# Kernel tuning notes

Measured on AMD Instinct MI355X. Metric: run time of the kernel, lower is better.

Reference implementation:

```python
import jax, jax.numpy as jnp
import numpy as np

N_BLOCKS = 64
BLOCK = 64
IN_SIZE = N_BLOCKS * BLOCK   # 4096
OUT_SIZE = N_BLOCKS * BLOCK  # 4096
EPS = 1e-6


def _masks():
    # block id per row/col (uniform block sizes)
    rb = np.repeat(np.arange(N_BLOCKS), BLOCK)
    cb = np.repeat(np.arange(N_BLOCKS), BLOCK)
    tree_mask = (rb[:, None] == cb[None, :]).astype(np.float32)    # block diagonal
    breeze_mask = (rb[:, None] < cb[None, :]).astype(np.float32)   # strict block upper-triangular
    return jnp.asarray(tree_mask), jnp.asarray(breeze_mask)


def setup_inputs() -> dict:
    key = jax.random.key(0)
    k1, k2, k3, k4 = jax.random.split(key, 4)
    x = jax.random.normal(k1, (8192, IN_SIZE), dtype=jnp.float32)
    x_init = jax.random.normal(k2, (8192, OUT_SIZE), dtype=jnp.float32)
    # inc_mode='no strict': treeWeights = sqrt(|randn| / sqrt(in_size/z_dim))
    tw = jnp.sqrt(jnp.abs(jax.random.normal(k3, (IN_SIZE, OUT_SIZE), dtype=jnp.float32))
                  / np.sqrt(IN_SIZE / N_BLOCKS))
    bbw = jax.random.normal(k4, (IN_SIZE, OUT_SIZE), dtype=jnp.float32) / np.sqrt(IN_SIZE)
    return {"x": x, "x_init": x_init, "treeWeights": tw, "breezeBiasWeights": bbw}


def reference(x, x_init, treeWeights, breezeBiasWeights):
    tree_mask, breeze_mask = _masks()
    # 'no strict': real weights are elementwise square (monotone-increasing, non-strict)
    tree_matrix = (treeWeights * treeWeights) * tree_mask          # [in, out]
    breeze_bias = x @ (breezeBiasWeights * breeze_mask)            # [B, out]
    h = x @ tree_matrix + x_init + breeze_bias                     # [B, out]
    # ActNorm-style data-dependent init (first call: bias/scale from batch stats)
    tree_bias = jax.lax.stop_gradient(jnp.mean(h, axis=0))         # [out]
    std = jax.lax.stop_gradient(jnp.std(h, axis=0))                # [out]
    tree_scale = jnp.sqrt(1.0 / (std + EPS))                       # stored scale; applied squared
    z = (h - tree_bias) * (tree_scale * tree_scale)
    return jax.nn.sigmoid(z)
```

## Files before the change

### kernel.cpp

```cpp
#include <hip/hip_runtime.h>
#include <stdint.h>


#define BATCH 8192
#define DIM   4096

typedef __bf16 v8bf __attribute__((ext_vector_type(8)));
typedef float  v4f  __attribute__((ext_vector_type(4)));

__device__ __forceinline__ unsigned short f2bf(float f) {
  unsigned int u = __float_as_uint(f);
  u += 0x7fffu + ((u >> 16) & 1u);
  return (unsigned short)(u >> 16);
}
__device__ __forceinline__ float bf2f(unsigned int h16) {
  return __uint_as_float(h16 << 16);
}

__device__ __forceinline__ void async_copy16(const void* g, void* l) {
  __builtin_amdgcn_global_load_lds(
      (__attribute__((address_space(1))) void*)g,
      (__attribute__((address_space(3))) void*)l, 16, 0, 0);
}

__global__ __launch_bounds__(256) void cvt_x_bf16(const float4* __restrict__ in,
                                                  uint4* __restrict__ out) {
  int i = blockIdx.x * 256 + threadIdx.x;
  float4 a = in[2 * i], b = in[2 * i + 1];
  uint4 o;
  o.x = (unsigned)f2bf(a.x) | ((unsigned)f2bf(a.y) << 16);
  o.y = (unsigned)f2bf(a.z) | ((unsigned)f2bf(a.w) << 16);
  o.z = (unsigned)f2bf(b.x) | ((unsigned)f2bf(b.y) << 16);
  o.w = (unsigned)f2bf(b.z) | ((unsigned)f2bf(b.w) << 16);
  out[i] = o;
}

__global__ __launch_bounds__(256) void build_Mt(const float* __restrict__ tw,
                                                const float* __restrict__ bbw,
                                                unsigned short* __restrict__ Mt) {
  const int kt = blockIdx.x, nt = blockIdx.y;
  const int t = threadIdx.x;
  const int jj = t & 63, i0 = t >> 6;
  __shared__ float tile[64 * 65];
  if (kt <= nt) {
    const bool diag = (kt == nt);
    const float* S = diag ? tw : bbw;
    #pragma unroll
    for (int r = 0; r < 16; ++r) {
      int i = i0 + r * 4;
      float v = S[(size_t)(kt * 64 + i) * DIM + nt * 64 + jj];
      tile[i * 65 + jj] = diag ? v * v : v;
    }
    __syncthreads();
    #pragma unroll
    for (int r = 0; r < 16; ++r) {
      int nl = i0 + r * 4;
      Mt[(size_t)(nt * 64 + nl) * DIM + kt * 64 + jj] = f2bf(tile[jj * 65 + nl]);
    }
  } else {
    #pragma unroll
    for (int r = 0; r < 16; ++r) {
      int nl = i0 + r * 4;
      Mt[(size_t)(nt * 64 + nl) * DIM + kt * 64 + jj] = 0;
    }
  }
}

__global__ __launch_bounds__(256) void gemm_tree(
    const unsigned short* __restrict__ Xb,
    const unsigned short* __restrict__ Mt,
    const float* __restrict__ Xi,
    unsigned short* __restrict__ H,
    float* __restrict__ colsum,
    float* __restrict__ colsumsq) {
  __shared__ unsigned short As[128 * 64];
  __shared__ unsigned short Bs[128 * 64];

  const int bid = (int)blockIdx.x;
  const int jc = 31 - (bid >> 6);
  const int bm = bid & 63;
  const int tid = threadIdx.x;
  const int wave = tid >> 6, lane = tid & 63;
  const int wm = (wave & 1) * 64, wn = (wave >> 1) * 64;
  const int lr = lane & 15, quad = lane >> 4;

  v4f acc[4][4];
  #pragma unroll
  for (int mi = 0; mi < 4; ++mi)
    #pragma unroll
    for (int ni = 0; ni < 4; ++ni) acc[mi][ni] = {0.f, 0.f, 0.f, 0.f};

  const int Kend = (jc + 1) * 128;
  const int srow = lane >> 3;
  const int scol = ((lane & 7) ^ srow) * 8;

  for (int k0 = 0; k0 < Kend; k0 += 64) {
    #pragma unroll
    for (int r = 0; r < 4; ++r) {
      int seg = wave * 4 + r;
      int row = seg * 8 + srow;
      const unsigned short* ga = Xb + (size_t)(bm * 128 + row) * DIM + (k0 + scol);
      const unsigned short* gb = Mt + (size_t)(jc * 128 + row) * DIM + (k0 + scol);
      async_copy16(ga, &As[seg * 512]);
      async_copy16(gb, &Bs[seg * 512]);
    }
    __syncthreads();
    #pragma unroll
    for (int kk = 0; kk < 2; ++kk) {
      const int sw = ((kk * 4 + quad) ^ (lr & 7)) * 8;
      v8bf a[4], b[4];
      #pragma unroll
      for (int mi = 0; mi < 4; ++mi)
        a[mi] = *(const v8bf*)&As[(wm + mi * 16 + lr) * 64 + sw];
      #pragma unroll
      for (int ni = 0; ni < 4; ++ni)
        b[ni] = *(const v8bf*)&Bs[(wn + ni * 16 + lr) * 64 + sw];
      #pragma unroll
      for (int mi = 0; mi < 4; ++mi)
        #pragma unroll
        for (int ni = 0; ni < 4; ++ni)
          acc[mi][ni] = __builtin_amdgcn_mfma_f32_16x16x32_bf16(
              a[mi], b[ni], acc[mi][ni], 0, 0, 0);
    }
    __syncthreads();
  }

  const int colT = jc * 128 + wn + lr;
  const int rowT = bm * 128 + wm + quad * 4;
  #pragma unroll
  for (int ni = 0; ni < 4; ++ni) {
    int col = colT + ni * 16;
    float s = 0.f, sq = 0.f;
    #pragma unroll
    for (int mi = 0; mi < 4; ++mi) {
      int row = rowT + mi * 16;
      #pragma unroll
      for (int r = 0; r < 4; ++r) {
        size_t idx = (size_t)(row + r) * DIM + col;
        float h = acc[mi][ni][r] + Xi[idx];
        H[idx] = f2bf(h);
        s += h;
        sq += h * h;
      }
    }
    s += __shfl_xor(s, 16);  s += __shfl_xor(s, 32);
    sq += __shfl_xor(sq, 16); sq += __shfl_xor(sq, 32);
    if (quad == 0) {
      atomicAdd(&colsum[col], s);
      atomicAdd(&colsumsq[col], sq);
    }
  }
}

__global__ __launch_bounds__(256) void finalize_stats(
    const float* __restrict__ colsum, const float* __restrict__ colsumsq,
    float* __restrict__ mean, float* __restrict__ scale) {
  int i = blockIdx.x * 256 + threadIdx.x;
  float m = colsum[i] * (1.0f / BATCH);
  float var = fmaxf(colsumsq[i] * (1.0f / BATCH) - m * m, 0.0f);
  mean[i] = m;
  scale[i] = 1.0f / (sqrtf(var) + 1e-6f);
}

__global__ __launch_bounds__(256) void norm_sigmoid(
    const uint4* __restrict__ H, const float* __restrict__ mean,
    const float* __restrict__ scale, float4* __restrict__ out) {
  int i = blockIdx.x * 256 + threadIdx.x;
  int cg = (i & 511) << 3;
  uint4 h = H[i];
  float4 m0 = *(const float4*)&mean[cg],  m1 = *(const float4*)&mean[cg + 4];
  float4 s0 = *(const float4*)&scale[cg], s1 = *(const float4*)&scale[cg + 4];
  float hv[8];
  hv[0] = bf2f(h.x & 0xffffu); hv[1] = bf2f(h.x >> 16);
  hv[2] = bf2f(h.y & 0xffffu); hv[3] = bf2f(h.y >> 16);
  hv[4] = bf2f(h.z & 0xffffu); hv[5] = bf2f(h.z >> 16);
  hv[6] = bf2f(h.w & 0xffffu); hv[7] = bf2f(h.w >> 16);
  float mm[8] = {m0.x, m0.y, m0.z, m0.w, m1.x, m1.y, m1.z, m1.w};
  float ss[8] = {s0.x, s0.y, s0.z, s0.w, s1.x, s1.y, s1.z, s1.w};
  #pragma unroll
  for (int j = 0; j < 8; ++j) {
    float z = (hv[j] - mm[j]) * ss[j];
    hv[j] = 1.0f / (1.0f + __expf(-z));
  }
  out[2 * i]     = make_float4(hv[0], hv[1], hv[2], hv[3]);
  out[2 * i + 1] = make_float4(hv[4], hv[5], hv[6], hv[7]);
}

extern "C" void kernel_launch(void* const* d_in, const int* in_sizes, int n_in,
                              void* d_out, int out_size, void* d_ws, size_t ws_size,
                              hipStream_t stream) {
  const float* x      = (const float*)d_in[0];
  const float* x_init = (const float*)d_in[1];
  const float* tw     = (const float*)d_in[2];
  const float* bbw    = (const float*)d_in[3];
  float* out = (float*)d_out;

  char* ws = (char*)d_ws;
  unsigned short* Xb = (unsigned short*)(ws);
  unsigned short* Mt = (unsigned short*)(ws + (size_t)67108864);
  unsigned short* H  = (unsigned short*)(ws + (size_t)100663296);
  float* colsum   = (float*)(ws + (size_t)167772160);
  float* colsumsq = (float*)(ws + (size_t)167772160 + 16384);
  float* mean     = (float*)(ws + (size_t)167772160 + 32768);
  float* scale    = (float*)(ws + (size_t)167772160 + 49152);

  hipMemsetAsync(colsum, 0, 32768, stream);

  cvt_x_bf16<<<(BATCH * DIM / 8 + 255) / 256, 256, 0, stream>>>(
      (const float4*)x, (uint4*)Xb);
  build_Mt<<<dim3(64, 64), 256, 0, stream>>>(tw, bbw, Mt);
  gemm_tree<<<2048, 256, 0, stream>>>(Xb, Mt, x_init, H, colsum, colsumsq);
  finalize_stats<<<16, 256, 0, stream>>>(colsum, colsumsq, mean, scale);
  norm_sigmoid<<<(BATCH * DIM / 8 + 255) / 256, 256, 0, stream>>>(
      (const uint4*)H, mean, scale, (float4*)out);
}
```

Baseline: 599.0 us.

## Double-buffer 256x256 GEMM tiles with paired triangular jobs and fused prep kernel

Rewrites the triangular GEMM to use 256x256 tiles with 8 waves and 32 accumulators per wave, and double-buffers the LDS loads so the next K tile is prefetched while MFMAs run. Each of the 256 workgroups takes two complementary column strips (jc and 15-jc) so every block does the same total K work. The bf16 conversion and weight-matrix build kernels are merged into one launch. The larger tiles raise register and LDS pressure, and a grid of only 256 blocks may leave some compute units idle.

```diff
diff --git a/kernel.cpp b/kernel.cpp
--- a/kernel.cpp
+++ b/kernel.cpp
@@ -23,131 +23,177 @@
       (__attribute__((address_space(3))) void*)l, 16, 0, 0);
 }
 
-__global__ __launch_bounds__(256) void cvt_x_bf16(const float4* __restrict__ in,
-                                                  uint4* __restrict__ out) {
-  int i = blockIdx.x * 256 + threadIdx.x;
-  float4 a = in[2 * i], b = in[2 * i + 1];
-  uint4 o;
-  o.x = (unsigned)f2bf(a.x) | ((unsigned)f2bf(a.y) << 16);
-  o.y = (unsigned)f2bf(a.z) | ((unsigned)f2bf(a.w) << 16);
-  o.z = (unsigned)f2bf(b.x) | ((unsigned)f2bf(b.y) << 16);
-  o.w = (unsigned)f2bf(b.z) | ((unsigned)f2bf(b.w) << 16);
-  out[i] = o;
-}
-
-__global__ __launch_bounds__(256) void build_Mt(const float* __restrict__ tw,
-                                                const float* __restrict__ bbw,
-                                                unsigned short* __restrict__ Mt) {
-  const int kt = blockIdx.x, nt = blockIdx.y;
-  const int t = threadIdx.x;
-  const int jj = t & 63, i0 = t >> 6;
+__global__ __launch_bounds__(256) void prep(
+    const float4* __restrict__ x, uint4* __restrict__ Xb,
+    const float* __restrict__ tw, const float* __restrict__ bbw,
+    unsigned short* __restrict__ Mt) {
+  const int b = (int)blockIdx.x;
+  const int t = (int)threadIdx.x;
   __shared__ float tile[64 * 65];
-  if (kt <= nt) {
-    const bool diag = (kt == nt);
-    const float* S = diag ? tw : bbw;
-    #pragma unroll
-    for (int r = 0; r < 16; ++r) {
-      int i = i0 + r * 4;
-      float v = S[(size_t)(kt * 64 + i) * DIM + nt * 64 + jj];
-      tile[i * 65 + jj] = diag ? v * v : v;
-    }
-    __syncthreads();
-    #pragma unroll
-    for (int r = 0; r < 16; ++r) {
-      int nl = i0 + r * 4;
-      Mt[(size_t)(nt * 64 + nl) * DIM + kt * 64 + jj] = f2bf(tile[jj * 65 + nl]);
-    }
+  if (b < 16384) {
+    int i = b * 256 + t;
+    float4 a = x[2 * i], c = x[2 * i + 1];
+    uint4 o;
+    o.x = (unsigned)f2bf(a.x) | ((unsigned)f2bf(a.y) << 16);
+    o.y = (unsigned)f2bf(a.z) | ((unsigned)f2bf(a.w) << 16);
+    o.z = (unsigned)f2bf(c.x) | ((unsigned)f2bf(c.y) << 16);
+    o.w = (unsigned)f2bf(c.z) | ((unsigned)f2bf(c.w) << 16);
+    Xb[i] = o;
   } else {
-    #pragma unroll
-    for (int r = 0; r < 16; ++r) {
-      int nl = i0 + r * 4;
-      Mt[(size_t)(nt * 64 + nl) * DIM + kt * 64 + jj] = 0;
+    const int bb = b - 16384;
+    const int kt = bb & 63, nt = bb >> 6;
+    const int jj = t & 63, i0 = t >> 6;
+    if (kt <= nt) {
+      const bool diag = (kt == nt);
+      const float* S = diag ? tw : bbw;
+      #pragma unroll
+      for (int r = 0; r < 16; ++r) {
+        int i = i0 + r * 4;
+        float v = S[(size_t)(kt * 64 + i) * DIM + nt * 64 + jj];
+        tile[i * 65 + jj] = diag ? v * v : v;
+      }
+      __syncthreads();
+      #pragma unroll
+      for (int r = 0; r < 16; ++r) {
+        int nl = i0 + r * 4;
+        Mt[(size_t)(nt * 64 + nl) * DIM + kt * 64 + jj] = f2bf(tile[jj * 65 + nl]);
+      }
+    } else {
+      #pragma unroll
+      for (int r = 0; r < 16; ++r) {
+        int nl = i0 + r * 4;
+        Mt[(size_t)(nt * 64 + nl) * DIM + kt * 64 + jj] = 0;
+      }
     }
   }
 }
 
-__global__ __launch_bounds__(256) void gemm_tree(
+__global__ __launch_bounds__(512, 2) void gemm_tree(
     const unsigned short* __restrict__ Xb,
     const unsigned short* __restrict__ Mt,
     const float* __restrict__ Xi,
     unsigned short* __restrict__ H,
     float* __restrict__ colsum,
     float* __restrict__ colsumsq) {
-  __shared__ unsigned short As[128 * 64];
-  __shared__ unsigned short Bs[128 * 64];
-
-  const int bid = (int)blockIdx.x;
-  const int jc = 31 - (bid >> 6);
-  const int bm = bid & 63;
-  const int tid = threadIdx.x;
+  __shared__ unsigned short As[2 * 16384];
+  __shared__ unsigned short Bs[2 * 16384];
+
+  const int b = (int)blockIdx.x;
+  const int p = b >> 5;
+  const int bm = b & 31;
+  const int tid = (int)threadIdx.x;
   const int wave = tid >> 6, lane = tid & 63;
-  const int wm = (wave & 1) * 64, wn = (wave >> 1) * 64;
+  const int wm = wave >> 2, wn = wave & 3;
   const int lr = lane & 15, quad = lane >> 4;
-
-  v4f acc[4][4];
-  #pragma unroll
-  for (int mi = 0; mi < 4; ++mi)
-    #pragma unroll
-    for (int ni = 0; ni < 4; ++ni) acc[mi][ni] = {0.f, 0.f, 0.f, 0.f};
-
-  const int Kend = (jc + 1) * 128;
   const int srow = lane >> 3;
   const int scol = ((lane & 7) ^ srow) * 8;
 
-  for (int k0 = 0; k0 < Kend; k0 += 64) {
+  const size_t abase = (size_t)(bm * 256 + wave * 8 + srow) * DIM + scol;
+
+  for (int job = 0; job < 2; ++job) {
+    const int jc = job ? p : 15 - p;
+    const int ntiles = (jc + 1) * 4;
+    const size_t bbase = (size_t)(jc * 256 + wave * 8 + srow) * DIM + scol;
+
+    v4f acc[8][4];
+    #pragma unroll
+    for (int mi = 0; mi < 8; ++mi)
+      #pragma unroll
+      for (int ni = 0; ni < 4; ++ni) acc[mi][ni] = {0.f, 0.f, 0.f, 0.f};
+
     #pragma unroll
     for (int r = 0; r < 4; ++r) {
-      int seg = wave * 4 + r;
-      int row = seg * 8 + srow;
-      const unsigned short* ga = Xb + (size_t)(bm * 128 + row) * DIM + (k0 + scol);
-      const unsigned short* gb = Mt + (size_t)(jc * 128 + row) * DIM + (k0 + scol);
-      async_copy16(ga, &As[seg * 512]);
-      async_copy16(gb, &Bs[seg * 512]);
-    }
-    __syncthreads();
+      async_copy16(Xb + abase + (size_t)(r * 64) * DIM, &As[(r * 8 + wave) * 512]);
+      async_copy16(Mt + bbase + (size_t)(r * 64) * DIM, &Bs[(r * 8 + wave) * 512]);
+    }
+
+    for (int t = 0; t < ntiles; ++t) {
+      const unsigned short* Ac = &As[(t & 1) * 16384];
+      const unsigned short* Bc = &Bs[(t & 1) * 16384];
+      const int nb = ((t + 1) & 1) * 16384;
+      const size_t nk = (size_t)(t + 1) * 64;
+      const bool pre = (t + 1 < ntiles);
+
+      if (pre) {
+        #pragma unroll
+        for (int r = 0; r < 2; ++r) {
+          async_copy16(Xb + abase + (size_t)(r * 64) * DIM + nk,
+                       &As[nb + (r * 8 + wave) * 512]);
+          async_copy16(Mt + bbase + (size_t)(r * 64) * DIM + nk,
+                       &Bs[nb + (r * 8 + wave) * 512]);
+        }
+        asm volatile("s_waitcnt vmcnt(4)" ::: "memory");
+      } else {
+        asm volatile("s_waitcnt vmcnt(0)" ::: "memory");
+      }
+      __builtin_amdgcn_s_barrier();
+      __builtin_amdgcn_sched_barrier(0);
+
+      v8bf bfr[4][2];
+      #pragma unroll
+      for (int ni = 0; ni < 4; ++ni)
+        #pragma unroll
+        for (int kk = 0; kk < 2; ++kk)
+          bfr[ni][kk] = *(const v8bf*)&Bc[(wn * 64 + ni * 16 + lr) * 64 +
+                                          (((kk * 4 + quad) ^ (lr & 7)) * 8)];
+
+      #pragma unroll
+      for (int q = 0; q < 4; ++q) {
+        v8bf afr[2][2];
+        #pragma unroll
+        for (int m2 = 0; m2 < 2; ++m2)
+          #pragma unroll
+          for (int kk = 0; kk < 2; ++kk)
+            afr[m2][kk] = *(const v8bf*)&Ac[(wm * 128 + (q * 2 + m2) * 16 + lr) * 64 +
+                                            (((kk * 4 + quad) ^ (lr & 7)) * 8)];
+        if (pre && q < 2) {
+          const int r = q + 2;
+          async_copy16(Xb + abase + (size_t)(r * 64) * DIM + nk,
+                       &As[nb + (r * 8 + wave) * 512]);
+          async_copy16(Mt + bbase + (size_t)(r * 64) * DIM + nk,
+                       &Bs[nb + (r * 8 + wave) * 512]);
+        }
+        __builtin_amdgcn_s_barrier();
+        __builtin_amdgcn_sched_barrier(0);
+        __builtin_amdgcn_s_setprio(1);
+        #pragma unroll
+        for (int kk = 0; kk < 2; ++kk)
+          #pragma unroll
+          for (int m2 = 0; m2 < 2; ++m2)
+            #pragma unroll
+            for (int ni = 0; ni < 4; ++ni)
+              acc[q * 2 + m2][ni] = __builtin_amdgcn_mfma_f32_16x16x32_bf16(
+                  afr[m2][kk], bfr[ni][kk], acc[q * 2 + m2][ni], 0, 0, 0);
+        __builtin_amdgcn_s_setprio(0);
+        __builtin_amdgcn_s_barrier();
+        __builtin_amdgcn_sched_barrier(0);
+      }
+    }
+
+    const int colT = jc * 256 + wn * 64 + lr;
+    const int rowT = bm * 256 + wm * 128 + quad * 4;
     #pragma unroll
-    for (int kk = 0; kk < 2; ++kk) {
-      const int sw = ((kk * 4 + quad) ^ (lr & 7)) * 8;
-      v8bf a[4], b[4];
-      #pragma unroll
-      for (int mi = 0; mi < 4; ++mi)
-        a[mi] = *(const v8bf*)&As[(wm + mi * 16 + lr) * 64 + sw];
-      #pragma unroll
-      for (int ni = 0; ni < 4; ++ni)
-        b[ni] = *(const v8bf*)&Bs[(wn + ni * 16 + lr) * 64 + sw];
-      #pragma unroll
-      for (int mi = 0; mi < 4; ++mi)
-        #pragma unroll
-        for (int ni = 0; ni < 4; ++ni)
-          acc[mi][ni] = __builtin_amdgcn_mfma_f32_16x16x32_bf16(
-              a[mi], b[ni], acc[mi][ni], 0, 0, 0);
-    }
-    __syncthreads();
-  }
-
-  const int colT = jc * 128 + wn + lr;
-  const int rowT = bm * 128 + wm + quad * 4;
-  #pragma unroll
-  for (int ni = 0; ni < 4; ++ni) {
-    int col = colT + ni * 16;
-    float s = 0.f, sq = 0.f;
-    #pragma unroll
-    for (int mi = 0; mi < 4; ++mi) {
-      int row = rowT + mi * 16;
-      #pragma unroll
-      for (int r = 0; r < 4; ++r) {
-        size_t idx = (size_t)(row + r) * DIM + col;
-        float h = acc[mi][ni][r] + Xi[idx];
-        H[idx] = f2bf(h);
-        s += h;
-        sq += h * h;
-      }
-    }
-    s += __shfl_xor(s, 16);  s += __shfl_xor(s, 32);
-    sq += __shfl_xor(sq, 16); sq += __shfl_xor(sq, 32);
-    if (quad == 0) {
-      atomicAdd(&colsum[col], s);
-      atomicAdd(&colsumsq[col], sq);
+    for (int ni = 0; ni < 4; ++ni) {
+      const int col = colT + ni * 16;
+      float s = 0.f, sq = 0.f;
+      #pragma unroll
+      for (int mi = 0; mi < 8; ++mi) {
+        const int row = rowT + mi * 16;
+        #pragma unroll
+        for (int r = 0; r < 4; ++r) {
+          size_t idx = (size_t)(row + r) * DIM + col;
+          float h = acc[mi][ni][r] + Xi[idx];
+          H[idx] = f2bf(h);
+          s += h;
+          sq += h * h;
+        }
+      }
+      s += __shfl_xor(s, 16);  s += __shfl_xor(s, 32);
+      sq += __shfl_xor(sq, 16); sq += __shfl_xor(sq, 32);
+      if (quad == 0) {
+        atomicAdd(&colsum[col], s);
+        atomicAdd(&colsumsq[col], sq);
+      }
     }
   }
 }
@@ -206,10 +252,8 @@
 
   hipMemsetAsync(colsum, 0, 32768, stream);
 
-  cvt_x_bf16<<<(BATCH * DIM / 8 + 255) / 256, 256, 0, stream>>>(
-      (const float4*)x, (uint4*)Xb);
-  build_Mt<<<dim3(64, 64), 256, 0, stream>>>(tw, bbw, Mt);
-  gemm_tree<<<2048, 256, 0, stream>>>(Xb, Mt, x_init, H, colsum, colsumsq);
+  prep<<<20480, 256, 0, stream>>>((const float4*)x, (uint4*)Xb, tw, bbw, Mt);
+  gemm_tree<<<256, 512, 0, stream>>>(Xb, Mt, x_init, H, colsum, colsumsq);
   finalize_stats<<<16, 256, 0, stream>>>(colsum, colsumsq, mean, scale);
   norm_sigmoid<<<(BATCH * DIM / 8 + 255) / 256, 256, 0, stream>>>(
       (const uint4*)H, mean, scale, (float4*)out);
```

New measurement: 661.6 us. 10.4% more time.

## Double-buffer GEMM LDS loads, pair triangular column tiles per block, merge prep kernels

Applied to the files above, without the earlier changes.

The GEMM kernel now double-buffers the A/B tiles in LDS, so the async global-to-LDS copies for the next K step are issued while MFMAs run on the current buffer. Each block processes two column tiles (jc and 31-jc) so that every block does the same amount of triangular work, with half as many blocks. The bf16 conversion of x and the construction of Mt are merged into a single launch. LDS use doubles, which may reduce occupancy, and 1024 blocks may leave part of the GPU idle near the tail.

```diff
diff --git a/kernel.cpp b/kernel.cpp
--- a/kernel.cpp
+++ b/kernel.cpp
@@ -23,45 +23,47 @@
       (__attribute__((address_space(3))) void*)l, 16, 0, 0);
 }
 
-__global__ __launch_bounds__(256) void cvt_x_bf16(const float4* __restrict__ in,
-                                                  uint4* __restrict__ out) {
-  int i = blockIdx.x * 256 + threadIdx.x;
-  float4 a = in[2 * i], b = in[2 * i + 1];
-  uint4 o;
-  o.x = (unsigned)f2bf(a.x) | ((unsigned)f2bf(a.y) << 16);
-  o.y = (unsigned)f2bf(a.z) | ((unsigned)f2bf(a.w) << 16);
-  o.z = (unsigned)f2bf(b.x) | ((unsigned)f2bf(b.y) << 16);
-  o.w = (unsigned)f2bf(b.z) | ((unsigned)f2bf(b.w) << 16);
-  out[i] = o;
-}
-
-__global__ __launch_bounds__(256) void build_Mt(const float* __restrict__ tw,
-                                                const float* __restrict__ bbw,
-                                                unsigned short* __restrict__ Mt) {
-  const int kt = blockIdx.x, nt = blockIdx.y;
-  const int t = threadIdx.x;
-  const int jj = t & 63, i0 = t >> 6;
+__global__ __launch_bounds__(256) void prep(
+    const float4* __restrict__ x, uint4* __restrict__ Xb,
+    const float* __restrict__ tw, const float* __restrict__ bbw,
+    unsigned short* __restrict__ Mt) {
+  const int b = (int)blockIdx.x;
+  const int t = (int)threadIdx.x;
   __shared__ float tile[64 * 65];
-  if (kt <= nt) {
-    const bool diag = (kt == nt);
-    const float* S = diag ? tw : bbw;
-    #pragma unroll
-    for (int r = 0; r < 16; ++r) {
-      int i = i0 + r * 4;
-      float v = S[(size_t)(kt * 64 + i) * DIM + nt * 64 + jj];
-      tile[i * 65 + jj] = diag ? v * v : v;
-    }
-    __syncthreads();
-    #pragma unroll
-    for (int r = 0; r < 16; ++r) {
-      int nl = i0 + r * 4;
-      Mt[(size_t)(nt * 64 + nl) * DIM + kt * 64 + jj] = f2bf(tile[jj * 65 + nl]);
-    }
+  if (b < 16384) {
+    int i = b * 256 + t;
+    float4 a = x[2 * i], c = x[2 * i + 1];
+    uint4 o;
+    o.x = (unsigned)f2bf(a.x) | ((unsigned)f2bf(a.y) << 16);
+    o.y = (unsigned)f2bf(a.z) | ((unsigned)f2bf(a.w) << 16);
+    o.z = (unsigned)f2bf(c.x) | ((unsigned)f2bf(c.y) << 16);
+    o.w = (unsigned)f2bf(c.z) | ((unsigned)f2bf(c.w) << 16);
+    Xb[i] = o;
   } else {
-    #pragma unroll
-    for (int r = 0; r < 16; ++r) {
-      int nl = i0 + r * 4;
-      Mt[(size_t)(nt * 64 + nl) * DIM + kt * 64 + jj] = 0;
+    const int bb = b - 16384;
+    const int kt = bb & 63, nt = bb >> 6;
+    const int jj = t & 63, i0 = t >> 6;
+    if (kt <= nt) {
+      const bool diag = (kt == nt);
+      const float* S = diag ? tw : bbw;
+      #pragma unroll
+      for (int r = 0; r < 16; ++r) {
+        int i = i0 + r * 4;
+        float v = S[(size_t)(kt * 64 + i) * DIM + nt * 64 + jj];
+        tile[i * 65 + jj] = diag ? v * v : v;
+      }
+      __syncthreads();
+      #pragma unroll
+      for (int r = 0; r < 16; ++r) {
+        int nl = i0 + r * 4;
+        Mt[(size_t)(nt * 64 + nl) * DIM + kt * 64 + jj] = f2bf(tile[jj * 65 + nl]);
+      }
+    } else {
+      #pragma unroll
+      for (int r = 0; r < 16; ++r) {
+        int nl = i0 + r * 4;
+        Mt[(size_t)(nt * 64 + nl) * DIM + kt * 64 + jj] = 0;
+      }
     }
   }
 }
@@ -73,81 +75,101 @@
     unsigned short* __restrict__ H,
     float* __restrict__ colsum,
     float* __restrict__ colsumsq) {
-  __shared__ unsigned short As[128 * 64];
-  __shared__ unsigned short Bs[128 * 64];
-
-  const int bid = (int)blockIdx.x;
-  const int jc = 31 - (bid >> 6);
-  const int bm = bid & 63;
-  const int tid = threadIdx.x;
+  __shared__ unsigned short As[2 * 8192];
+  __shared__ unsigned short Bs[2 * 8192];
+
+  const int b = (int)blockIdx.x;
+  const int p = b >> 6;
+  const int bm = b & 63;
+  const int tid = (int)threadIdx.x;
   const int wave = tid >> 6, lane = tid & 63;
   const int wm = (wave & 1) * 64, wn = (wave >> 1) * 64;
   const int lr = lane & 15, quad = lane >> 4;
-
-  v4f acc[4][4];
-  #pragma unroll
-  for (int mi = 0; mi < 4; ++mi)
-    #pragma unroll
-    for (int ni = 0; ni < 4; ++ni) acc[mi][ni] = {0.f, 0.f, 0.f, 0.f};
-
-  const int Kend = (jc + 1) * 128;
   const int srow = lane >> 3;
   const int scol = ((lane & 7) ^ srow) * 8;
 
-  for (int k0 = 0; k0 < Kend; k0 += 64) {
+  for (int job = 0; job < 2; ++job) {
+    const int jc = job ? p : 31 - p;
+    const int nsteps = (jc + 1) * 2;
+    const size_t arow0 = (size_t)bm * 128;
+    const size_t brow0 = (size_t)jc * 128;
+
+    v4f acc[4][4];
+    #pragma unroll
+    for (int mi = 0; mi < 4; ++mi)
+      #pragma unroll
+      for (int ni = 0; ni < 4; ++ni) acc[mi][ni] = {0.f, 0.f, 0.f, 0.f};
+
     #pragma unroll
     for (int r = 0; r < 4; ++r) {
       int seg = wave * 4 + r;
       int row = seg * 8 + srow;
-      const unsigned short* ga = Xb + (size_t)(bm * 128 + row) * DIM + (k0 + scol);
-      const unsigned short* gb = Mt + (size_t)(jc * 128 + row) * DIM + (k0 + scol);
-      async_copy16(ga, &As[seg * 512]);
-      async_copy16(gb, &Bs[seg * 512]);
-    }
-    __syncthreads();
+      async_copy16(Xb + (arow0 + row) * DIM + scol, &As[seg * 512]);
+      async_copy16(Mt + (brow0 + row) * DIM + scol, &Bs[seg * 512]);
+    }
+    asm volatile("s_waitcnt vmcnt(0)" ::: "memory");
+    __builtin_amdgcn_s_barrier();
+    __builtin_amdgcn_sched_barrier(0);
+
+    for (int t = 0; t < nsteps; ++t) {
+      const int cur = (t & 1) * 8192;
+      if (t + 1 < nsteps) {
+        const int nxt = ((t + 1) & 1) * 8192;
+        const size_t nk = (size_t)(t + 1) * 64 + scol;
+        #pragma unroll
+        for (int r = 0; r < 4; ++r) {
+          int seg = wave * 4 + r;
+          int row = seg * 8 + srow;
+          async_copy16(Xb + (arow0 + row) * DIM + nk, &As[nxt + seg * 512]);
+          async_copy16(Mt + (brow0 + row) * DIM + nk, &Bs[nxt + seg * 512]);
+        }
+      }
+      #pragma unroll
+      for (int kk = 0; kk < 2; ++kk) {
+        const int sw = ((kk * 4 + quad) ^ (lr & 7)) * 8;
+        v8bf a[4], bb[4];
+        #pragma unroll
+        for (int mi = 0; mi < 4; ++mi)
+          a[mi] = *(const v8bf*)&As[cur + (wm + mi * 16 + lr) * 64 + sw];
+        #pragma unroll
+        for (int ni = 0; ni < 4; ++ni)
+          bb[ni] = *(const v8bf*)&Bs[cur + (wn + ni * 16 + lr) * 64 + sw];
+        #pragma unroll
+        for (int mi = 0; mi < 4; ++mi)
+          #pragma unroll
+          for (int ni = 0; ni < 4; ++ni)
+            acc[mi][ni] = __builtin_amdgcn_mfma_f32_16x16x32_bf16(
+                a[mi], bb[ni], acc[mi][ni], 0, 0, 0);
+      }
+      asm volatile("s_waitcnt vmcnt(0)" ::: "memory");
+      __builtin_amdgcn_s_barrier();
+      __builtin_amdgcn_sched_barrier(0);
+    }
+
+    const int colT = jc * 128 + wn + lr;
+    const int rowT = bm * 128 + wm + quad * 4;
     #pragma unroll
-    for (int kk = 0; kk < 2; ++kk) {
-      const int sw = ((kk * 4 + quad) ^ (lr & 7)) * 8;
-      v8bf a[4], b[4];
-      #pragma unroll
-      for (int mi = 0; mi < 4; ++mi)
-        a[mi] = *(const v8bf*)&As[(wm + mi * 16 + lr) * 64 + sw];
-      #pragma unroll
-      for (int ni = 0; ni < 4; ++ni)
-        b[ni] = *(const v8bf*)&Bs[(wn + ni * 16 + lr) * 64 + sw];
-      #pragma unroll
-      for (int mi = 0; mi < 4; ++mi)
-        #pragma unroll
-        for (int ni = 0; ni < 4; ++ni)
-          acc[mi][ni] = __builtin_amdgcn_mfma_f32_16x16x32_bf16(
-              a[mi], b[ni], acc[mi][ni], 0, 0, 0);
-    }
-    __syncthreads();
-  }
-
-  const int colT = jc * 128 + wn + lr;
-  const int rowT = bm * 128 + wm + quad * 4;
-  #pragma unroll
-  for (int ni = 0; ni < 4; ++ni) {
-    int col = colT + ni * 16;
-    float s = 0.f, sq = 0.f;
-    #pragma unroll
-    for (int mi = 0; mi < 4; ++mi) {
-      int row = rowT + mi * 16;
-      #pragma unroll
-      for (int r = 0; r < 4; ++r) {
-        size_t idx = (size_t)(row + r) * DIM + col;
-        float h = acc[mi][ni][r] + Xi[idx];
-        H[idx] = f2bf(h);
-        s += h;
-        sq += h * h;
-      }
-    }
-    s += __shfl_xor(s, 16);  s += __shfl_xor(s, 32);
-    sq += __shfl_xor(sq, 16); sq += __shfl_xor(sq, 32);
-    if (quad == 0) {
-      atomicAdd(&colsum[col], s);
-      atomicAdd(&colsumsq[col], sq);
+    for (int ni = 0; ni < 4; ++ni) {
+      int col = colT + ni * 16;
+      float s = 0.f, sq = 0.f;
+      #pragma unroll
+      for (int mi = 0; mi < 4; ++mi) {
+        int row = rowT + mi * 16;
+        #pragma unroll
+        for (int r = 0; r < 4; ++r) {
+          size_t idx = (size_t)(row + r) * DIM + col;
+          float h = acc[mi][ni][r] + Xi[idx];
+          H[idx] = f2bf(h);
+          s += h;
+          sq += h * h;
+        }
+      }
+      s += __shfl_xor(s, 16);  s += __shfl_xor(s, 32);
+      sq += __shfl_xor(sq, 16); sq += __shfl_xor(sq, 32);
+      if (quad == 0) {
+        atomicAdd(&colsum[col], s);
+        atomicAdd(&colsumsq[col], sq);
+      }
     }
   }
 }
@@ -206,10 +228,8 @@
 
   hipMemsetAsync(colsum, 0, 32768, stream);
 
-  cvt_x_bf16<<<(BATCH * DIM / 8 + 255) / 256, 256, 0, stream>>>(
-      (const float4*)x, (uint4*)Xb);
-  build_Mt<<<dim3(64, 64), 256, 0, stream>>>(tw, bbw, Mt);
-  gemm_tree<<<2048, 256, 0, stream>>>(Xb, Mt, x_init, H, colsum, colsumsq);
+  prep<<<20480, 256, 0, stream>>>((const float4*)x, (uint4*)Xb, tw, bbw, Mt);
+  gemm_tree<<<1024, 256, 0, stream>>>(Xb, Mt, x_init, H, colsum, colsumsq);
   finalize_stats<<<16, 256, 0, stream>>>(colsum, colsumsq, mean, scale);
   norm_sigmoid<<<(BATCH * DIM / 8 + 255) / 256, 256, 0, stream>>>(
       (const uint4*)H, mean, scale, (float4*)out);
```

Result: slower. 704.6 us (+17.6%).
